# Performance work log

Hardware: AMD Instinct MI355X
Metric: run time of the kernel (lower is better)

The kernel has to match this reference:

```python
import jax, jax.numpy as jnp
import numpy as np

B, T, D, H = 256, 2048, 64, 64

def setup_inputs() -> dict:
    key = jax.random.key(0)
    ks = jax.random.split(key, 9)
    s_in = 1.0 / np.sqrt(D)
    s_rec = 1.0 / np.sqrt(H)
    return {
        "lstm_input": jax.random.normal(ks[0], (B, T, D), dtype=jnp.float32),
        "inputs_state": jax.random.normal(ks[1], (B, H), dtype=jnp.float32),
        # LSTM kernel/recurrent_kernel/bias, Keras gate order [i, f, c, o]
        "W": jax.random.normal(ks[2], (D, 4 * H), dtype=jnp.float32) * s_in,
        "U": jax.random.normal(ks[3], (H, 4 * H), dtype=jnp.float32) * s_rec,
        "b": jax.random.normal(ks[4], (4 * H,), dtype=jnp.float32) * 0.05,
        # Dense(1) heads
        "w_gamma": jax.random.normal(ks[5], (H, 1), dtype=jnp.float32) * s_rec,
        "b_gamma": jax.random.normal(ks[6], (1,), dtype=jnp.float32) * 0.05,
        "w_beta": jax.random.normal(ks[7], (H, 1), dtype=jnp.float32) * s_rec,
        "b_beta": jax.random.normal(ks[8], (1,), dtype=jnp.float32) * 0.05,
    }

def reference(lstm_input, inputs_state, W, U, b, w_gamma, b_gamma, w_beta, b_beta):
    # Keras LSTM(64, activation='sigmoid'): recurrent_activation=sigmoid (gates),
    # activation=sigmoid (candidate + cell output, replacing the usual tanh).
    # get_initial_state(inputs_state) -> zero h0/c0 (only batch size is used).
    sig = jax.nn.sigmoid
    # Precompute input projections for all timesteps: [B,T,4H]
    xz = jnp.einsum('btd,dg->btg', lstm_input, W) + b

    def step(carry, z_t):
        h, c = carry
        z = z_t + h @ U  # [B,4H]
        i, f, g, o = jnp.split(z, 4, axis=-1)
        c = sig(f) * c + sig(i) * sig(g)
        h = sig(o) * sig(c)
        return (h, c), None

    h0 = jnp.zeros((lstm_input.shape[0], H), dtype=lstm_input.dtype)
    c0 = jnp.zeros_like(h0)
    (h, _), _ = jax.lax.scan(step, (h0, c0), jnp.swapaxes(xz, 0, 1))

    gamma = h @ w_gamma + b_gamma  # [B,1]
    beta = h @ w_beta + b_beta     # [B,1]
    return (gamma, beta)
```

## Files before the change

### kernel.cpp

```cpp
#include <hip/hip_runtime.h>


typedef _Float16 f16;
typedef f16  half8 __attribute__((ext_vector_type(8)));
typedef float f32x4 __attribute__((ext_vector_type(4)));

constexpr int Bsz = 256;
constexpr int Tn  = 2048;
constexpr int Dn  = 64;
constexpr int G4  = 256;
constexpr int BPB = 4;
constexpr int HSTR = 160;

__device__ __forceinline__ float sigmoidf_fast(float z) {
    return __builtin_amdgcn_rcpf(1.0f + __expf(-z));
}

__global__ __launch_bounds__(256, 1) void lstm_film_mfma(
    const float* __restrict__ x,
    const float* __restrict__ W,
    const float* __restrict__ U,
    const float* __restrict__ bias,
    const float* __restrict__ wg, const float* __restrict__ bgam,
    const float* __restrict__ wb, const float* __restrict__ bbet,
    float* __restrict__ out)
{
    __shared__ __align__(16) char hbuf[2][BPB * HSTR];

    const int tid  = threadIdx.x;
    const int w    = tid >> 6;
    const int l    = tid & 63;
    const int lrow = l & 15;
    const int kgrp = l >> 4;

    half8 Bf[4][4];
#pragma unroll
    for (int kf = 0; kf < 4; ++kf) {
        const float* M = (kf < 2) ? U : W;
        const int krow0 = (kf & 1) * 32 + kgrp * 8;
#pragma unroll
        for (int q = 0; q < 4; ++q) {
            const int col = q * 64 + w * 16 + lrow;
#pragma unroll
            for (int j = 0; j < 8; ++j)
                Bf[kf][q][j] = (f16)M[(krow0 + j) * G4 + col];
        }
    }
    float bq[4];
#pragma unroll
    for (int q = 0; q < 4; ++q) bq[q] = bias[q * 64 + w * 16 + lrow];

    if (tid < (2 * BPB * HSTR) / 16) ((uint4*)hbuf)[tid] = uint4{0, 0, 0, 0};
    float c = 0.0f;

    const float* xlane = x + ((size_t)(blockIdx.x * BPB + (lrow >> 2)) * Tn
                              + (lrow & 3)) * Dn + kgrp * 8;

    const int rdA = (lrow >> 2) * HSTR + kgrp * 16;
    const int rdB = rdA + 64;
    const int wrb = (l >> 4) * HSTR + (w * 16 + lrow) * 2;

    const float wgj = wg[l], wbj = wb[l];
    const float bg0 = bgam[0], bb0 = bbet[0];

    __syncthreads();

#define XL(R, TB) do {                                                       \
        const float* p_ = xlane + (size_t)(TB) * (4 * Dn);                   \
        R[0] = *(const float4*)(p_);      R[1] = *(const float4*)(p_ + 4);   \
        R[2] = *(const float4*)(p_ + 32); R[3] = *(const float4*)(p_ + 36);  \
    } while (0)

    float4 RA[4], RB[4];
    XL(RA, 0); XL(RB, 1);

    f32x4 xzA0, xzA1, xzA2, xzA3, xzB0, xzB1, xzB2, xzB3;

#define XBLOCK(XZ, R, TBN) do {                                              \
        half8 af0, af1;                                                      \
        af0[0]=(f16)R[0].x; af0[1]=(f16)R[0].y; af0[2]=(f16)R[0].z;          \
        af0[3]=(f16)R[0].w; af0[4]=(f16)R[1].x; af0[5]=(f16)R[1].y;          \
        af0[6]=(f16)R[1].z; af0[7]=(f16)R[1].w;                              \
        af1[0]=(f16)R[2].x; af1[1]=(f16)R[2].y; af1[2]=(f16)R[2].z;          \
        af1[3]=(f16)R[2].w; af1[4]=(f16)R[3].x; af1[5]=(f16)R[3].y;          \
        af1[6]=(f16)R[3].z; af1[7]=(f16)R[3].w;                              \
        XL(R, TBN);                             \
        XZ##0 = f32x4{bq[0], bq[0], bq[0], bq[0]};                           \
        XZ##1 = f32x4{bq[1], bq[1], bq[1], bq[1]};                           \
        XZ##2 = f32x4{bq[2], bq[2], bq[2], bq[2]};                           \
        XZ##3 = f32x4{bq[3], bq[3], bq[3], bq[3]};                           \
        XZ##0 = __builtin_amdgcn_mfma_f32_16x16x32_f16(af0, Bf[2][0], XZ##0,0,0,0);\
        XZ##1 = __builtin_amdgcn_mfma_f32_16x16x32_f16(af0, Bf[2][1], XZ##1,0,0,0);\
        XZ##2 = __builtin_amdgcn_mfma_f32_16x16x32_f16(af0, Bf[2][2], XZ##2,0,0,0);\
        XZ##3 = __builtin_amdgcn_mfma_f32_16x16x32_f16(af0, Bf[2][3], XZ##3,0,0,0);\
        XZ##0 = __builtin_amdgcn_mfma_f32_16x16x32_f16(af1, Bf[3][0], XZ##0,0,0,0);\
        XZ##1 = __builtin_amdgcn_mfma_f32_16x16x32_f16(af1, Bf[3][1], XZ##1,0,0,0);\
        XZ##2 = __builtin_amdgcn_mfma_f32_16x16x32_f16(af1, Bf[3][2], XZ##2,0,0,0);\
        XZ##3 = __builtin_amdgcn_mfma_f32_16x16x32_f16(af1, Bf[3][3], XZ##3,0,0,0);\
    } while (0)

#define HSTEP(XZ, S, P) do {                                                 \
        asm volatile("s_waitcnt lgkmcnt(0)" ::: "memory");                   \
        __builtin_amdgcn_s_barrier();                                        \
        asm volatile("" ::: "memory");                                       \
        const char* hb = hbuf[P];                                            \
        half8 ah0 = *(const half8*)(hb + rdA);                               \
        half8 ah1 = *(const half8*)(hb + rdB);                               \
        const f32x4 zr = {0.f, 0.f, 0.f, 0.f};                               \
        f32x4 ha0 = __builtin_amdgcn_mfma_f32_16x16x32_f16(ah0, Bf[0][0], zr,0,0,0);\
        f32x4 ha1 = __builtin_amdgcn_mfma_f32_16x16x32_f16(ah0, Bf[0][1], zr,0,0,0);\
        f32x4 ha2 = __builtin_amdgcn_mfma_f32_16x16x32_f16(ah0, Bf[0][2], zr,0,0,0);\
        f32x4 ha3 = __builtin_amdgcn_mfma_f32_16x16x32_f16(ah0, Bf[0][3], zr,0,0,0);\
        f32x4 hb0 = __builtin_amdgcn_mfma_f32_16x16x32_f16(ah1, Bf[1][0], zr,0,0,0);\
        f32x4 hb1 = __builtin_amdgcn_mfma_f32_16x16x32_f16(ah1, Bf[1][1], zr,0,0,0);\
        f32x4 hb2 = __builtin_amdgcn_mfma_f32_16x16x32_f16(ah1, Bf[1][2], zr,0,0,0);\
        f32x4 hb3 = __builtin_amdgcn_mfma_f32_16x16x32_f16(ah1, Bf[1][3], zr,0,0,0);\
        const float zi = ha0[0] + hb0[0] + XZ##0[S];                         \
        const float zf = ha1[0] + hb1[0] + XZ##1[S];                         \
        const float zg = ha2[0] + hb2[0] + XZ##2[S];                         \
        const float zo = ha3[0] + hb3[0] + XZ##3[S];                         \
        const float gi = sigmoidf_fast(zi);                                  \
        const float gf = sigmoidf_fast(zf);                                  \
        const float gg = sigmoidf_fast(zg);                                  \
        const float go = sigmoidf_fast(zo);                                  \
        c = fmaf(gf, c, gi * gg);                                            \
        const float hh = go * sigmoidf_fast(c);                              \
        *(f16*)(hbuf[(P) ^ 1] + wrb) = (f16)hh;                              \
    } while (0)

    constexpr int NTB = Tn / 4;
    for (int tb = 0; tb < NTB; tb += 2) {
        const int tbn0 = tb + 2 < NTB ? tb + 2 : NTB - 1;
        const int tbn1 = tb + 3 < NTB ? tb + 3 : NTB - 1;
        XBLOCK(xzA, RA, tbn0);
        HSTEP(xzA, 0, 0); HSTEP(xzA, 1, 1); HSTEP(xzA, 2, 0); HSTEP(xzA, 3, 1);
        XBLOCK(xzB, RB, tbn1);
        HSTEP(xzB, 0, 0); HSTEP(xzB, 1, 1); HSTEP(xzB, 2, 0); HSTEP(xzB, 3, 1);
    }
#undef HSTEP
#undef XBLOCK
#undef XL

    __syncthreads();

    {
        const float hv = (float)*(const f16*)(hbuf[0] + w * HSTR + l * 2);
        float vg = hv * wgj, vb = hv * wbj;
#pragma unroll
        for (int off = 32; off > 0; off >>= 1) {
            vg += __shfl_xor(vg, off, 64);
            vb += __shfl_xor(vb, off, 64);
        }
        if (l == 0) {
            out[blockIdx.x * BPB + w]       = vg + bg0;
            out[Bsz + blockIdx.x * BPB + w] = vb + bb0;
        }
    }
}

extern "C" void kernel_launch(void* const* d_in, const int* in_sizes, int n_in,
                              void* d_out, int out_size, void* d_ws, size_t ws_size,
                              hipStream_t stream) {
    const float* x    = (const float*)d_in[0];
    const float* W    = (const float*)d_in[2];
    const float* U    = (const float*)d_in[3];
    const float* bias = (const float*)d_in[4];
    const float* wg   = (const float*)d_in[5];
    const float* bgam = (const float*)d_in[6];
    const float* wb   = (const float*)d_in[7];
    const float* bbet = (const float*)d_in[8];
    float* out = (float*)d_out;

    lstm_film_mfma<<<Bsz / BPB, 256, 0, stream>>>(x, W, U, bias,
                                                  wg, bgam, wb, bbet, out);
}
```

Measured before the change: 504.3 us.

## Fold log2e scaling into weights, merge sigmoid reciprocals, pipeline x-projection ahead

Pre-scales W, U and the bias by -log2(e) so each gate sigmoid becomes a raw exp2 plus reciprocal, and merges products of sigmoids into a single reciprocal. The x-projection result is now fed as the MFMA accumulator instead of being added after the MFMAs. The x-projection block for the next four timesteps is issued one block earlier, between the barrier and the recurrent MFMAs, to shorten the serial per-step critical path. Scaling the weights before the f16 conversion slightly changes rounding, and the product-of-denominators reciprocal could overflow to inf for very negative pre-activations.

```diff
diff --git a/kernel.cpp b/kernel.cpp
--- a/kernel.cpp
+++ b/kernel.cpp
@@ -11,10 +11,6 @@
 constexpr int G4  = 256;
 constexpr int BPB = 4;
 constexpr int HSTR = 160;
-
-__device__ __forceinline__ float sigmoidf_fast(float z) {
-    return __builtin_amdgcn_rcpf(1.0f + __expf(-z));
-}
 
 __global__ __launch_bounds__(256, 1) void lstm_film_mfma(
     const float* __restrict__ x,
@@ -33,6 +29,8 @@
     const int lrow = l & 15;
     const int kgrp = l >> 4;
 
+    const float NK = -1.44269504f;
+
     half8 Bf[4][4];
 #pragma unroll
     for (int kf = 0; kf < 4; ++kf) {
@@ -43,12 +41,12 @@
             const int col = q * 64 + w * 16 + lrow;
 #pragma unroll
             for (int j = 0; j < 8; ++j)
-                Bf[kf][q][j] = (f16)M[(krow0 + j) * G4 + col];
+                Bf[kf][q][j] = (f16)(M[(krow0 + j) * G4 + col] * NK);
         }
     }
     float bq[4];
 #pragma unroll
-    for (int q = 0; q < 4; ++q) bq[q] = bias[q * 64 + w * 16 + lrow];
+    for (int q = 0; q < 4; ++q) bq[q] = bias[q * 64 + w * 16 + lrow] * NK;
 
     if (tid < (2 * BPB * HSTR) / 16) ((uint4*)hbuf)[tid] = uint4{0, 0, 0, 0};
     float c = 0.0f;
@@ -99,45 +97,65 @@
         XZ##3 = __builtin_amdgcn_mfma_f32_16x16x32_f16(af1, Bf[3][3], XZ##3,0,0,0);\
     } while (0)
 
-#define HSTEP(XZ, S, P) do {                                                 \
+#define HSTEP_PRE(P)                                                         \
         asm volatile("s_waitcnt lgkmcnt(0)" ::: "memory");                   \
         __builtin_amdgcn_s_barrier();                                        \
         asm volatile("" ::: "memory");                                       \
-        const char* hb = hbuf[P];                                            \
-        half8 ah0 = *(const half8*)(hb + rdA);                               \
-        half8 ah1 = *(const half8*)(hb + rdB);                               \
-        const f32x4 zr = {0.f, 0.f, 0.f, 0.f};                               \
-        f32x4 ha0 = __builtin_amdgcn_mfma_f32_16x16x32_f16(ah0, Bf[0][0], zr,0,0,0);\
-        f32x4 ha1 = __builtin_amdgcn_mfma_f32_16x16x32_f16(ah0, Bf[0][1], zr,0,0,0);\
-        f32x4 ha2 = __builtin_amdgcn_mfma_f32_16x16x32_f16(ah0, Bf[0][2], zr,0,0,0);\
-        f32x4 ha3 = __builtin_amdgcn_mfma_f32_16x16x32_f16(ah0, Bf[0][3], zr,0,0,0);\
-        f32x4 hb0 = __builtin_amdgcn_mfma_f32_16x16x32_f16(ah1, Bf[1][0], zr,0,0,0);\
-        f32x4 hb1 = __builtin_amdgcn_mfma_f32_16x16x32_f16(ah1, Bf[1][1], zr,0,0,0);\
-        f32x4 hb2 = __builtin_amdgcn_mfma_f32_16x16x32_f16(ah1, Bf[1][2], zr,0,0,0);\
-        f32x4 hb3 = __builtin_amdgcn_mfma_f32_16x16x32_f16(ah1, Bf[1][3], zr,0,0,0);\
-        const float zi = ha0[0] + hb0[0] + XZ##0[S];                         \
-        const float zf = ha1[0] + hb1[0] + XZ##1[S];                         \
-        const float zg = ha2[0] + hb2[0] + XZ##2[S];                         \
-        const float zo = ha3[0] + hb3[0] + XZ##3[S];                         \
-        const float gi = sigmoidf_fast(zi);                                  \
-        const float gf = sigmoidf_fast(zf);                                  \
-        const float gg = sigmoidf_fast(zg);                                  \
-        const float go = sigmoidf_fast(zo);                                  \
-        c = fmaf(gf, c, gi * gg);                                            \
-        const float hh = go * sigmoidf_fast(c);                              \
+        const char* hb_ = hbuf[P];                                           \
+        half8 ah0_ = *(const half8*)(hb_ + rdA);                             \
+        half8 ah1_ = *(const half8*)(hb_ + rdB);
+
+#define HSTEP_POST(XZ, S, P) do {                                            \
+        f32x4 c0 = XZ##0; c0[0] = XZ##0[S];                                  \
+        f32x4 c1 = XZ##1; c1[0] = XZ##1[S];                                  \
+        f32x4 c2 = XZ##2; c2[0] = XZ##2[S];                                  \
+        f32x4 c3 = XZ##3; c3[0] = XZ##3[S];                                  \
+        c0 = __builtin_amdgcn_mfma_f32_16x16x32_f16(ah0_, Bf[0][0], c0,0,0,0);\
+        c1 = __builtin_amdgcn_mfma_f32_16x16x32_f16(ah0_, Bf[0][1], c1,0,0,0);\
+        c2 = __builtin_amdgcn_mfma_f32_16x16x32_f16(ah0_, Bf[0][2], c2,0,0,0);\
+        c3 = __builtin_amdgcn_mfma_f32_16x16x32_f16(ah0_, Bf[0][3], c3,0,0,0);\
+        c0 = __builtin_amdgcn_mfma_f32_16x16x32_f16(ah1_, Bf[1][0], c0,0,0,0);\
+        c1 = __builtin_amdgcn_mfma_f32_16x16x32_f16(ah1_, Bf[1][1], c1,0,0,0);\
+        c2 = __builtin_amdgcn_mfma_f32_16x16x32_f16(ah1_, Bf[1][2], c2,0,0,0);\
+        c3 = __builtin_amdgcn_mfma_f32_16x16x32_f16(ah1_, Bf[1][3], c3,0,0,0);\
+                         \
+        const float ei = __builtin_amdgcn_exp2f(c0[0]);                      \
+        const float ef = __builtin_amdgcn_exp2f(c1[0]);                      \
+        const float eg = __builtin_amdgcn_exp2f(c2[0]);                      \
+        const float eo = __builtin_amdgcn_exp2f(c3[0]);                      \
+        const float sf  = __builtin_amdgcn_rcpf(1.0f + ef);                  \
+        const float sig = __builtin_amdgcn_rcpf((1.0f + ei) * (1.0f + eg));  \
+        c = fmaf(sf, c, sig);                                                \
+        const float ec = __builtin_amdgcn_exp2f(c * NK);                     \
+        const float hh = __builtin_amdgcn_rcpf((1.0f + eo) * (1.0f + ec));   \
         *(f16*)(hbuf[(P) ^ 1] + wrb) = (f16)hh;                              \
     } while (0)
 
+    XBLOCK(xzA, RA, 2);
+
     constexpr int NTB = Tn / 4;
     for (int tb = 0; tb < NTB; tb += 2) {
-        const int tbn0 = tb + 2 < NTB ? tb + 2 : NTB - 1;
-        const int tbn1 = tb + 3 < NTB ? tb + 3 : NTB - 1;
-        XBLOCK(xzA, RA, tbn0);
-        HSTEP(xzA, 0, 0); HSTEP(xzA, 1, 1); HSTEP(xzA, 2, 0); HSTEP(xzA, 3, 1);
-        XBLOCK(xzB, RB, tbn1);
-        HSTEP(xzB, 0, 0); HSTEP(xzB, 1, 1); HSTEP(xzB, 2, 0); HSTEP(xzB, 3, 1);
+        const int tbn0 = tb + 3 < NTB ? tb + 3 : NTB - 1;
+        const int tbn1 = tb + 4 < NTB ? tb + 4 : NTB - 1;
+        {
+            HSTEP_PRE(0)
+            XBLOCK(xzB, RB, tbn0);
+            HSTEP_POST(xzA, 0, 0);
+        }
+        { HSTEP_PRE(1) HSTEP_POST(xzA, 1, 1); }
+        { HSTEP_PRE(0) HSTEP_POST(xzA, 2, 0); }
+        { HSTEP_PRE(1) HSTEP_POST(xzA, 3, 1); }
+        {
+            HSTEP_PRE(0)
+            XBLOCK(xzA, RA, tbn1);
+            HSTEP_POST(xzB, 0, 0);
+        }
+        { HSTEP_PRE(1) HSTEP_POST(xzB, 1, 1); }
+        { HSTEP_PRE(0) HSTEP_POST(xzB, 2, 0); }
+        { HSTEP_PRE(1) HSTEP_POST(xzB, 3, 1); }
     }
-#undef HSTEP
+#undef HSTEP_PRE
+#undef HSTEP_POST
 #undef XBLOCK
 #undef XL
 
```

New measurement: 461.1 us. 8.6% less time.
